# Kernel optimization log

Hardware: AMD Instinct MI355X
Metric: run time of the kernel (lower is better)

Reference implementation:

```python
import jax, jax.numpy as jnp
import numpy as np

N = 100000
E = 1600000
IN_C, HID_C, OUT_C = 64, 64, 16


def setup_inputs() -> dict:
    key = jax.random.key(0)
    k1, k2, k3, k4, k5 = jax.random.split(key, 5)
    x = jax.random.normal(k1, (N, IN_C), dtype=jnp.float32)
    edge_index = jax.random.randint(k2, (2, E), 0, N, dtype=jnp.int64)
    # Glorot-style init like PyG GCNConv
    W1 = jax.random.normal(k3, (IN_C, HID_C), dtype=jnp.float32) * (1.0 / np.sqrt(IN_C))
    b1 = jnp.zeros((HID_C,), dtype=jnp.float32)
    W2 = jax.random.normal(k4, (HID_C, OUT_C), dtype=jnp.float32) * (1.0 / np.sqrt(HID_C))
    b2 = jnp.zeros((OUT_C,), dtype=jnp.float32)
    return {"x": x, "edge_index": edge_index, "W1": W1, "b1": b1, "W2": W2, "b2": b2}


def _gcn_conv(h, src, dst, norm, W, b, n_nodes):
    # h: [N, F_in] -> linear transform first (PyG order), then normalized aggregation
    h = h @ W  # [N, F_out]
    msgs = h[src] * norm[:, None]          # gather + scale, [E+N, F_out]
    out = jax.ops.segment_sum(msgs, dst, num_segments=n_nodes)  # scatter-add
    return out + b


def reference(x, edge_index, W1, b1, W2, b2):
    n = x.shape[0]
    loop = jnp.arange(n, dtype=edge_index.dtype)
    src = jnp.concatenate([edge_index[0], loop])  # add self-loops
    dst = jnp.concatenate([edge_index[1], loop])
    # symmetric normalization D^{-1/2} (A+I) D^{-1/2}
    deg = jax.ops.segment_sum(jnp.ones_like(dst, dtype=x.dtype), dst, num_segments=n)
    dinv = jnp.where(deg > 0, jax.lax.rsqrt(deg), 0.0)
    norm = dinv[src] * dinv[dst]  # [E+N]

    h = jax.nn.relu(_gcn_conv(x, src, dst, norm, W1, b1, n))
    # dropout is identity in eval mode
    return _gcn_conv(h, src, dst, norm, W2, b2, n)
```

## Files before the change

### kernel.cpp

```cpp
#include <hip/hip_runtime.h>


namespace {
constexpr int BLK = 256;
constexpr int NPB = 256;
constexpr int PCHUNK = 2048;
constexpr int STRIDE = 5120;

__device__ inline float bf2f(unsigned short h) {
    union { unsigned u; float f; } v; v.u = (unsigned)h << 16; return v.f;
}
__device__ inline unsigned short f2bf(float f) {
    union { float f; unsigned u; } v; v.f = f;
    unsigned r = (v.u + 0x7FFFu + ((v.u >> 16) & 1u)) >> 16;
    return (unsigned short)r;
}
__device__ inline unsigned pack2bf(float a, float b) {
    return (unsigned)f2bf(a) | ((unsigned)f2bf(b) << 16);
}

__global__ __launch_bounds__(BLK) void k_zero(int* __restrict__ p, int n) {
    int i = blockIdx.x * BLK + threadIdx.x;
    if (i < n) p[i] = 0;
}

__global__ __launch_bounds__(BLK) void k_part(const int* __restrict__ src,
                                              const int* __restrict__ dst,
                                              int* __restrict__ bcnt,
                                              unsigned* __restrict__ packed,
                                              int e, int nb) {
    __shared__ int sdst[PCHUNK];
    __shared__ int hist[1024];
    __shared__ int base[1024];
    int t = threadIdx.x;
    int chunk0 = blockIdx.x * PCHUNK;
    if (chunk0 >= e) return;
    int lim = min(PCHUNK, e - chunk0);
    for (int i = t; i < nb; i += BLK) hist[i] = 0;
    __syncthreads();
    for (int i = t; i < lim; i += BLK) {
        int d = dst[chunk0 + i];
        sdst[i] = d;
        atomicAdd(&hist[d >> 8], 1);
    }
    __syncthreads();
    for (int i = t; i < nb; i += BLK) {
        int c = hist[i];
        base[i] = c ? (i * STRIDE + atomicAdd(&bcnt[i], c)) : 0;
        hist[i] = 0;
    }
    __syncthreads();
    for (int i = t; i < lim; i += BLK) {
        int d = sdst[i];
        int b = d >> 8;
        int r = atomicAdd(&hist[b], 1);
        packed[base[b] + r] = ((unsigned)src[chunk0 + i] << 8) | (unsigned)(d & 255);
    }
}

__global__ __launch_bounds__(BLK) void k_sort(const unsigned* __restrict__ packed,
                                              const int* __restrict__ bcnt,
                                              int* __restrict__ ssrc,
                                              int* __restrict__ rowbeg,
                                              int* __restrict__ rowcnt,
                                              float* __restrict__ dinv, int n) {
    __shared__ int cnt[NPB];
    __shared__ int offs[NPB];
    int b = blockIdx.x;
    int t = threadIdx.x;
    int regionBase = b * STRIDE;
    int ecnt = bcnt[b];
    cnt[t] = 0;
    __syncthreads();
    for (int i = t; i < ecnt; i += BLK) atomicAdd(&cnt[packed[regionBase + i] & 255u], 1);
    __syncthreads();
    int v = cnt[t];
    offs[t] = v;
    __syncthreads();
    for (int off = 1; off < NPB; off <<= 1) {
        int x = (t >= off) ? offs[t - off] : 0;
        __syncthreads();
        offs[t] += x;
        __syncthreads();
    }
    int myoff = offs[t] - v;
    int node = (b << 8) + t;
    if (node < n) {
        rowbeg[node] = regionBase + myoff;
        rowcnt[node] = v;
        dinv[node] = rsqrtf((float)(v + 1));
    }
    __syncthreads();
    cnt[t] = regionBase + myoff;
    __syncthreads();
    for (int i = t; i < ecnt; i += BLK) {
        unsigned p = packed[regionBase + i];
        int pos = atomicAdd(&cnt[p & 255u], 1);
        ssrc[pos] = (int)(p >> 8);
    }
}


__global__ __launch_bounds__(BLK) void k_gemm1(const float* __restrict__ x,
                                               const float* __restrict__ W1,
                                               const float* __restrict__ dinv,
                                               unsigned short* __restrict__ hhat, int n) {
    __shared__ float W[64 * 64];
    int t = threadIdx.x;
    #pragma unroll
    for (int i = 0; i < 16; ++i) W[t + BLK * i] = W1[t + BLK * i];
    __syncthreads();
    const int cg = t & 3;
    const int ng = t >> 2;
    const int node0 = blockIdx.x * 256 + ng * 4;
    const float* Wc = W + cg * 16;

    int nd[4];
    #pragma unroll
    for (int i = 0; i < 4; ++i) {
        int v = node0 + i;
        nd[i] = (v < n) ? v : (n - 1);
    }

    float4 acc[4][4];
    #pragma unroll
    for (int i = 0; i < 4; ++i)
        #pragma unroll
        for (int c = 0; c < 4; ++c) acc[i][c] = make_float4(0.f, 0.f, 0.f, 0.f);

    for (int k4 = 0; k4 < 16; ++k4) {
        float4 xv[4];
        #pragma unroll
        for (int i = 0; i < 4; ++i)
            xv[i] = ((const float4*)(x + (size_t)nd[i] * 64))[k4];
        #pragma unroll
        for (int kk = 0; kk < 4; ++kk) {
            const float4* wr = (const float4*)(Wc + (k4 * 4 + kk) * 64);
            float4 w0 = wr[0], w1 = wr[1], w2 = wr[2], w3 = wr[3];
            #pragma unroll
            for (int i = 0; i < 4; ++i) {
                float xa[4] = {xv[i].x, xv[i].y, xv[i].z, xv[i].w};
                float xs = xa[kk];
                acc[i][0].x = fmaf(xs, w0.x, acc[i][0].x);
                acc[i][0].y = fmaf(xs, w0.y, acc[i][0].y);
                acc[i][0].z = fmaf(xs, w0.z, acc[i][0].z);
                acc[i][0].w = fmaf(xs, w0.w, acc[i][0].w);
                acc[i][1].x = fmaf(xs, w1.x, acc[i][1].x);
                acc[i][1].y = fmaf(xs, w1.y, acc[i][1].y);
                acc[i][1].z = fmaf(xs, w1.z, acc[i][1].z);
                acc[i][1].w = fmaf(xs, w1.w, acc[i][1].w);
                acc[i][2].x = fmaf(xs, w2.x, acc[i][2].x);
                acc[i][2].y = fmaf(xs, w2.y, acc[i][2].y);
                acc[i][2].z = fmaf(xs, w2.z, acc[i][2].z);
                acc[i][2].w = fmaf(xs, w2.w, acc[i][2].w);
                acc[i][3].x = fmaf(xs, w3.x, acc[i][3].x);
                acc[i][3].y = fmaf(xs, w3.y, acc[i][3].y);
                acc[i][3].z = fmaf(xs, w3.z, acc[i][3].z);
                acc[i][3].w = fmaf(xs, w3.w, acc[i][3].w);
            }
        }
    }
    #pragma unroll
    for (int i = 0; i < 4; ++i) {
        int v = node0 + i;
        if (v < n) {
            float d = dinv[v];
            unsigned u0 = pack2bf(acc[i][0].x * d, acc[i][0].y * d);
            unsigned u1 = pack2bf(acc[i][0].z * d, acc[i][0].w * d);
            unsigned u2 = pack2bf(acc[i][1].x * d, acc[i][1].y * d);
            unsigned u3 = pack2bf(acc[i][1].z * d, acc[i][1].w * d);
            unsigned u4 = pack2bf(acc[i][2].x * d, acc[i][2].y * d);
            unsigned u5 = pack2bf(acc[i][2].z * d, acc[i][2].w * d);
            unsigned u6 = pack2bf(acc[i][3].x * d, acc[i][3].y * d);
            unsigned u7 = pack2bf(acc[i][3].z * d, acc[i][3].w * d);
            uint4* dst = (uint4*)(hhat + (size_t)v * 64 + cg * 16);
            dst[0] = make_uint4(u0, u1, u2, u3);
            dst[1] = make_uint4(u4, u5, u6, u7);
        }
    }
}

__global__ __launch_bounds__(BLK) void k_agg1(const unsigned short* __restrict__ hhat,
                                              const int* __restrict__ rowbeg,
                                              const int* __restrict__ rowcnt,
                                              const int* __restrict__ ssrc,
                                              const float* __restrict__ dinv,
                                              const float* __restrict__ b1,
                                              float* __restrict__ h1, int n) {
    int wid = __builtin_amdgcn_readfirstlane(
        (int)((blockIdx.x * BLK + threadIdx.x) >> 6));
    int lane = threadIdx.x & 63;
    if (wid >= n) return;
    int beg = rowbeg[wid];
    int cnt = rowcnt[wid];
    float a = bf2f(hhat[((size_t)wid << 6) + lane]);
    int e = 0;
    for (; e + 8 <= cnt; e += 8) {
        int s0 = ssrc[beg + e + 0], s1 = ssrc[beg + e + 1];
        int s2 = ssrc[beg + e + 2], s3 = ssrc[beg + e + 3];
        int s4 = ssrc[beg + e + 4], s5 = ssrc[beg + e + 5];
        int s6 = ssrc[beg + e + 6], s7 = ssrc[beg + e + 7];
        float v0 = bf2f(hhat[((size_t)s0 << 6) + lane]);
        float v1 = bf2f(hhat[((size_t)s1 << 6) + lane]);
        float v2 = bf2f(hhat[((size_t)s2 << 6) + lane]);
        float v3 = bf2f(hhat[((size_t)s3 << 6) + lane]);
        float v4 = bf2f(hhat[((size_t)s4 << 6) + lane]);
        float v5 = bf2f(hhat[((size_t)s5 << 6) + lane]);
        float v6 = bf2f(hhat[((size_t)s6 << 6) + lane]);
        float v7 = bf2f(hhat[((size_t)s7 << 6) + lane]);
        a += ((v0 + v1) + (v2 + v3)) + ((v4 + v5) + (v6 + v7));
    }
    if (e + 4 <= cnt) {
        int s0 = ssrc[beg + e + 0], s1 = ssrc[beg + e + 1];
        int s2 = ssrc[beg + e + 2], s3 = ssrc[beg + e + 3];
        float v0 = bf2f(hhat[((size_t)s0 << 6) + lane]);
        float v1 = bf2f(hhat[((size_t)s1 << 6) + lane]);
        float v2 = bf2f(hhat[((size_t)s2 << 6) + lane]);
        float v3 = bf2f(hhat[((size_t)s3 << 6) + lane]);
        a += (v0 + v1) + (v2 + v3);
        e += 4;
    }
    for (; e < cnt; ++e)
        a += bf2f(hhat[((size_t)ssrc[beg + e] << 6) + lane]);
    h1[((size_t)wid << 6) + lane] = fmaxf(fmaf(dinv[wid], a, b1[lane]), 0.f);
}

__global__ __launch_bounds__(BLK) void k_gemm2(const float* __restrict__ h1,
                                               const float* __restrict__ W2,
                                               const float* __restrict__ dinv,
                                               unsigned short* __restrict__ h2hat, int n) {
    __shared__ float W[64 * 16];
    int t = threadIdx.x;
    #pragma unroll
    for (int i = 0; i < 4; ++i) W[t + BLK * i] = W2[t + BLK * i];
    __syncthreads();
    int node = blockIdx.x * BLK + t;
    if (node >= n) return;
    const float4* hr = (const float4*)(h1 + (size_t)node * 64);
    float4 a0 = make_float4(0.f, 0.f, 0.f, 0.f);
    float4 a1 = a0, a2 = a0, a3 = a0;
    #pragma unroll 4
    for (int c4 = 0; c4 < 16; ++c4) {
        float4 h = hr[c4];
        #pragma unroll
        for (int kk = 0; kk < 4; ++kk) {
            float ha[4] = {h.x, h.y, h.z, h.w};
            float hv = ha[kk];
            const float4* wr = (const float4*)(W + (c4 * 4 + kk) * 16);
            float4 w0 = wr[0], w1 = wr[1], w2 = wr[2], w3 = wr[3];
            a0.x = fmaf(hv, w0.x, a0.x); a0.y = fmaf(hv, w0.y, a0.y);
            a0.z = fmaf(hv, w0.z, a0.z); a0.w = fmaf(hv, w0.w, a0.w);
            a1.x = fmaf(hv, w1.x, a1.x); a1.y = fmaf(hv, w1.y, a1.y);
            a1.z = fmaf(hv, w1.z, a1.z); a1.w = fmaf(hv, w1.w, a1.w);
            a2.x = fmaf(hv, w2.x, a2.x); a2.y = fmaf(hv, w2.y, a2.y);
            a2.z = fmaf(hv, w2.z, a2.z); a2.w = fmaf(hv, w2.w, a2.w);
            a3.x = fmaf(hv, w3.x, a3.x); a3.y = fmaf(hv, w3.y, a3.y);
            a3.z = fmaf(hv, w3.z, a3.z); a3.w = fmaf(hv, w3.w, a3.w);
        }
    }
    float d = dinv[node];
    uint4* dst = (uint4*)(h2hat + (size_t)node * 16);
    dst[0] = make_uint4(pack2bf(a0.x * d, a0.y * d), pack2bf(a0.z * d, a0.w * d),
                        pack2bf(a1.x * d, a1.y * d), pack2bf(a1.z * d, a1.w * d));
    dst[1] = make_uint4(pack2bf(a2.x * d, a2.y * d), pack2bf(a2.z * d, a2.w * d),
                        pack2bf(a3.x * d, a3.y * d), pack2bf(a3.z * d, a3.w * d));
}

__global__ __launch_bounds__(BLK) void k_agg2(const unsigned short* __restrict__ h2hat,
                                              const int* __restrict__ rowbeg,
                                              const int* __restrict__ rowcnt,
                                              const int* __restrict__ ssrc,
                                              const float* __restrict__ dinv,
                                              const float* __restrict__ b2,
                                              float* __restrict__ out, int n) {
    int wid = __builtin_amdgcn_readfirstlane(
        (int)((blockIdx.x * BLK + threadIdx.x) >> 6));
    int lane = threadIdx.x & 63;
    if (wid >= n) return;
    int q = lane >> 4;
    int c = lane & 15;
    int beg = rowbeg[wid];
    int cnt = rowcnt[wid];
    float a = 0.f;
    int e = q;
    for (; e + 4 < cnt; e += 8) {
        int sa = ssrc[beg + e];
        int sb = ssrc[beg + e + 4];
        float va = bf2f(h2hat[((size_t)sa << 4) + c]);
        float vb = bf2f(h2hat[((size_t)sb << 4) + c]);
        a += va + vb;
    }
    if (e < cnt) a += bf2f(h2hat[((size_t)ssrc[beg + e] << 4) + c]);
    a += __shfl_xor(a, 16, 64);
    a += __shfl_xor(a, 32, 64);
    if (q == 0) {
        float self = bf2f(h2hat[((size_t)wid << 4) + c]);
        out[((size_t)wid << 4) + c] = fmaf(dinv[wid], a + self, b2[c]);
    }
}

}

extern "C" void kernel_launch(void* const* d_in, const int* in_sizes, int n_in,
                              void* d_out, int out_size, void* d_ws, size_t ws_size,
                              hipStream_t stream) {
    const float* x  = (const float*)d_in[0];
    const int*   ei = (const int*)d_in[1];
    const float* W1 = (const float*)d_in[2];
    const float* b1 = (const float*)d_in[3];
    const float* W2 = (const float*)d_in[4];
    const float* b2 = (const float*)d_in[5];
    float* out = (float*)d_out;

    const int N = in_sizes[0] / 64;
    const int E = in_sizes[1] / 2;
    const int* src = ei;
    const int* dst = ei + E;
    const int nb = (N + NPB - 1) / NPB;

    char* ws = (char*)d_ws;
    size_t off = 0;
    auto alloc = [&](size_t bytes) -> char* {
        char* p = ws + off;
        off = (off + bytes + 255) & ~(size_t)255;
        return p;
    };
    int*            bcnt   = (int*)alloc(1024 * 4);
    int*            rowbeg = (int*)alloc((size_t)N * 4);
    int*            rowcnt = (int*)alloc((size_t)N * 4);
    float*          dinv   = (float*)alloc((size_t)N * 4);
    unsigned*       packed = (unsigned*)alloc((size_t)nb * STRIDE * 4);
    int*            ssrc   = (int*)alloc((size_t)nb * STRIDE * 4);
    unsigned short* hhat   = (unsigned short*)alloc((size_t)N * 64 * 2);
    float*          h1     = (float*)alloc((size_t)N * 64 * 4);
    unsigned short* h2hat  = (unsigned short*)alloc((size_t)N * 16 * 2);

    const int nb_n = (N + BLK - 1) / BLK;
    const int nchunks = (E + PCHUNK - 1) / PCHUNK;
    const int nb_w = (int)(((long long)N * 64 + BLK - 1) / BLK);

    k_zero<<<(nb + BLK - 1) / BLK, BLK, 0, stream>>>(bcnt, nb);
    k_part<<<nchunks, BLK, 0, stream>>>(src, dst, bcnt, packed, E, nb);
    k_sort<<<nb, BLK, 0, stream>>>(packed, bcnt, ssrc, rowbeg, rowcnt, dinv, N);

    k_gemm1<<<nb_n, BLK, 0, stream>>>(x, W1, dinv, hhat, N);
    k_agg1<<<nb_w, BLK, 0, stream>>>(hhat, rowbeg, rowcnt, ssrc, dinv, b1, h1, N);

    k_gemm2<<<nb_n, BLK, 0, stream>>>(h1, W2, dinv, h2hat, N);
    k_agg2<<<nb_w, BLK, 0, stream>>>(h2hat, rowbeg, rowcnt, ssrc, dinv, b2, out, N);
}
```

Before: 242.5 us.

## Widen aggregation loads to packed bf16 pairs, pad bucket counters, enlarge sort blocks

The two aggregation kernels now read two bf16 values per 32-bit load. agg1 splits the wave into two halves that each handle alternate edges, and agg2 uses eight slots of eight lanes. Both combine partial sums with cross-lane shuffles. Partition chunks grow fourfold, global bucket counters are padded to separate cache lines to reduce atomic contention, and the sort kernel runs 1024-thread blocks. These changes aim to cut gather instruction count and atomic hot spots, at the cost of extra shuffles, fewer partition blocks, and idle threads in the scan.

Measured after the change: 242.6 us. About the same (+0.0%).

```diff
diff --git a/kernel.cpp b/kernel.cpp
--- a/kernel.cpp
+++ b/kernel.cpp
@@ -4,11 +4,18 @@
 namespace {
 constexpr int BLK = 256;
 constexpr int NPB = 256;
-constexpr int PCHUNK = 2048;
+constexpr int PCHUNK = 8192;
 constexpr int STRIDE = 5120;
+constexpr int CPAD = 32;
 
 __device__ inline float bf2f(unsigned short h) {
     union { unsigned u; float f; } v; v.u = (unsigned)h << 16; return v.f;
+}
+__device__ inline float bfl(unsigned u) {
+    union { unsigned u; float f; } v; v.u = u << 16; return v.f;
+}
+__device__ inline float bfh(unsigned u) {
+    union { unsigned u; float f; } v; v.u = u & 0xFFFF0000u; return v.f;
 }
 __device__ inline unsigned short f2bf(float f) {
     union { float f; unsigned u; } v; v.f = f;
@@ -46,7 +53,7 @@
     __syncthreads();
     for (int i = t; i < nb; i += BLK) {
         int c = hist[i];
-        base[i] = c ? (i * STRIDE + atomicAdd(&bcnt[i], c)) : 0;
+        base[i] = c ? (i * STRIDE + atomicAdd(&bcnt[i * CPAD], c)) : 0;
         hist[i] = 0;
     }
     __syncthreads();
@@ -58,42 +65,47 @@
     }
 }
 
-__global__ __launch_bounds__(BLK) void k_sort(const unsigned* __restrict__ packed,
-                                              const int* __restrict__ bcnt,
-                                              int* __restrict__ ssrc,
-                                              int* __restrict__ rowbeg,
-                                              int* __restrict__ rowcnt,
-                                              float* __restrict__ dinv, int n) {
+__global__ __launch_bounds__(1024) void k_sort(const unsigned* __restrict__ packed,
+                                               const int* __restrict__ bcnt,
+                                               int* __restrict__ ssrc,
+                                               int* __restrict__ rowbeg,
+                                               int* __restrict__ rowcnt,
+                                               float* __restrict__ dinv, int n) {
     __shared__ int cnt[NPB];
     __shared__ int offs[NPB];
     int b = blockIdx.x;
     int t = threadIdx.x;
     int regionBase = b * STRIDE;
-    int ecnt = bcnt[b];
-    cnt[t] = 0;
-    __syncthreads();
-    for (int i = t; i < ecnt; i += BLK) atomicAdd(&cnt[packed[regionBase + i] & 255u], 1);
-    __syncthreads();
-    int v = cnt[t];
-    offs[t] = v;
+    int ecnt = bcnt[b * CPAD];
+    if (t < NPB) cnt[t] = 0;
+    __syncthreads();
+    for (int i = t; i < ecnt; i += 1024)
+        atomicAdd(&cnt[packed[regionBase + i] & 255u], 1);
+    __syncthreads();
+    if (t < NPB) offs[t] = cnt[t];
     __syncthreads();
     for (int off = 1; off < NPB; off <<= 1) {
-        int x = (t >= off) ? offs[t - off] : 0;
+        int x = 0;
+        if (t < NPB && t >= off) x = offs[t - off];
         __syncthreads();
-        offs[t] += x;
+        if (t < NPB) offs[t] += x;
         __syncthreads();
     }
-    int myoff = offs[t] - v;
-    int node = (b << 8) + t;
-    if (node < n) {
-        rowbeg[node] = regionBase + myoff;
-        rowcnt[node] = v;
-        dinv[node] = rsqrtf((float)(v + 1));
-    }
-    __syncthreads();
-    cnt[t] = regionBase + myoff;
-    __syncthreads();
-    for (int i = t; i < ecnt; i += BLK) {
+    int myoff = 0;
+    if (t < NPB) {
+        int v = cnt[t];
+        myoff = offs[t] - v;
+        int node = (b << 8) + t;
+        if (node < n) {
+            rowbeg[node] = regionBase + myoff;
+            rowcnt[node] = v;
+            dinv[node] = rsqrtf((float)(v + 1));
+        }
+    }
+    __syncthreads();
+    if (t < NPB) cnt[t] = regionBase + myoff;
+    __syncthreads();
+    for (int i = t; i < ecnt; i += 1024) {
         unsigned p = packed[regionBase + i];
         int pos = atomicAdd(&cnt[p & 255u], 1);
         ssrc[pos] = (int)(p >> 8);
@@ -180,7 +192,7 @@
     }
 }
 
-__global__ __launch_bounds__(BLK) void k_agg1(const unsigned short* __restrict__ hhat,
+__global__ __launch_bounds__(BLK) void k_agg1(const unsigned* __restrict__ hh,
                                               const int* __restrict__ rowbeg,
                                               const int* __restrict__ rowcnt,
                                               const int* __restrict__ ssrc,
@@ -191,38 +203,49 @@
         (int)((blockIdx.x * BLK + threadIdx.x) >> 6));
     int lane = threadIdx.x & 63;
     if (wid >= n) return;
+    int half = lane >> 5;
+    int cp = lane & 31;
     int beg = rowbeg[wid];
     int cnt = rowcnt[wid];
-    float a = bf2f(hhat[((size_t)wid << 6) + lane]);
+    float ax = 0.f, ay = 0.f;
+    if (half == 0) {
+        unsigned u = hh[((size_t)wid << 5) + cp];
+        ax = bfl(u); ay = bfh(u);
+    }
     int e = 0;
     for (; e + 8 <= cnt; e += 8) {
-        int s0 = ssrc[beg + e + 0], s1 = ssrc[beg + e + 1];
-        int s2 = ssrc[beg + e + 2], s3 = ssrc[beg + e + 3];
-        int s4 = ssrc[beg + e + 4], s5 = ssrc[beg + e + 5];
-        int s6 = ssrc[beg + e + 6], s7 = ssrc[beg + e + 7];
-        float v0 = bf2f(hhat[((size_t)s0 << 6) + lane]);
-        float v1 = bf2f(hhat[((size_t)s1 << 6) + lane]);
-        float v2 = bf2f(hhat[((size_t)s2 << 6) + lane]);
-        float v3 = bf2f(hhat[((size_t)s3 << 6) + lane]);
-        float v4 = bf2f(hhat[((size_t)s4 << 6) + lane]);
-        float v5 = bf2f(hhat[((size_t)s5 << 6) + lane]);
-        float v6 = bf2f(hhat[((size_t)s6 << 6) + lane]);
-        float v7 = bf2f(hhat[((size_t)s7 << 6) + lane]);
-        a += ((v0 + v1) + (v2 + v3)) + ((v4 + v5) + (v6 + v7));
-    }
-    if (e + 4 <= cnt) {
-        int s0 = ssrc[beg + e + 0], s1 = ssrc[beg + e + 1];
-        int s2 = ssrc[beg + e + 2], s3 = ssrc[beg + e + 3];
-        float v0 = bf2f(hhat[((size_t)s0 << 6) + lane]);
-        float v1 = bf2f(hhat[((size_t)s1 << 6) + lane]);
-        float v2 = bf2f(hhat[((size_t)s2 << 6) + lane]);
-        float v3 = bf2f(hhat[((size_t)s3 << 6) + lane]);
-        a += (v0 + v1) + (v2 + v3);
-        e += 4;
-    }
-    for (; e < cnt; ++e)
-        a += bf2f(hhat[((size_t)ssrc[beg + e] << 6) + lane]);
-    h1[((size_t)wid << 6) + lane] = fmaxf(fmaf(dinv[wid], a, b1[lane]), 0.f);
+        int i0 = beg + e + half;
+        int s0 = ssrc[i0];
+        int s1 = ssrc[i0 + 2];
+        int s2 = ssrc[i0 + 4];
+        int s3 = ssrc[i0 + 6];
+        unsigned u0 = hh[((size_t)s0 << 5) + cp];
+        unsigned u1 = hh[((size_t)s1 << 5) + cp];
+        unsigned u2 = hh[((size_t)s2 << 5) + cp];
+        unsigned u3 = hh[((size_t)s3 << 5) + cp];
+        ax += (bfl(u0) + bfl(u1)) + (bfl(u2) + bfl(u3));
+        ay += (bfh(u0) + bfh(u1)) + (bfh(u2) + bfh(u3));
+    }
+    for (; e + 2 <= cnt; e += 2) {
+        int s = ssrc[beg + e + half];
+        unsigned u = hh[((size_t)s << 5) + cp];
+        ax += bfl(u); ay += bfh(u);
+    }
+    if (e < cnt && half == 0) {
+        int s = ssrc[beg + e];
+        unsigned u = hh[((size_t)s << 5) + cp];
+        ax += bfl(u); ay += bfh(u);
+    }
+    ax += __shfl_xor(ax, 32, 64);
+    ay += __shfl_xor(ay, 32, 64);
+    if (half == 0) {
+        float d = dinv[wid];
+        float2 bb = ((const float2*)b1)[cp];
+        float2 o;
+        o.x = fmaxf(fmaf(d, ax, bb.x), 0.f);
+        o.y = fmaxf(fmaf(d, ay, bb.y), 0.f);
+        ((float2*)(h1 + ((size_t)wid << 6)))[cp] = o;
+    }
 }
 
 __global__ __launch_bounds__(BLK) void k_gemm2(const float* __restrict__ h1,
@@ -266,7 +289,7 @@
                         pack2bf(a3.x * d, a3.y * d), pack2bf(a3.z * d, a3.w * d));
 }
 
-__global__ __launch_bounds__(BLK) void k_agg2(const unsigned short* __restrict__ h2hat,
+__global__ __launch_bounds__(BLK) void k_agg2(const unsigned* __restrict__ h2,
                                               const int* __restrict__ rowbeg,
                                               const int* __restrict__ rowcnt,
                                               const int* __restrict__ ssrc,
@@ -277,25 +300,43 @@
         (int)((blockIdx.x * BLK + threadIdx.x) >> 6));
     int lane = threadIdx.x & 63;
     if (wid >= n) return;
-    int q = lane >> 4;
-    int c = lane & 15;
+    int slot = lane >> 3;
+    int u = lane & 7;
     int beg = rowbeg[wid];
     int cnt = rowcnt[wid];
-    float a = 0.f;
-    int e = q;
-    for (; e + 4 < cnt; e += 8) {
-        int sa = ssrc[beg + e];
-        int sb = ssrc[beg + e + 4];
-        float va = bf2f(h2hat[((size_t)sa << 4) + c]);
-        float vb = bf2f(h2hat[((size_t)sb << 4) + c]);
-        a += va + vb;
-    }
-    if (e < cnt) a += bf2f(h2hat[((size_t)ssrc[beg + e] << 4) + c]);
-    a += __shfl_xor(a, 16, 64);
-    a += __shfl_xor(a, 32, 64);
-    if (q == 0) {
-        float self = bf2f(h2hat[((size_t)wid << 4) + c]);
-        out[((size_t)wid << 4) + c] = fmaf(dinv[wid], a + self, b2[c]);
+    float ax = 0.f, ay = 0.f;
+    int e = 0;
+    for (; e + 16 <= cnt; e += 16) {
+        int i0 = beg + e + slot;
+        int s0 = ssrc[i0];
+        int s1 = ssrc[i0 + 8];
+        unsigned u0 = h2[((size_t)s0 << 3) + u];
+        unsigned u1 = h2[((size_t)s1 << 3) + u];
+        ax += bfl(u0) + bfl(u1);
+        ay += bfh(u0) + bfh(u1);
+    }
+    if (e + 8 <= cnt) {
+        int s = ssrc[beg + e + slot];
+        unsigned uu = h2[((size_t)s << 3) + u];
+        ax += bfl(uu); ay += bfh(uu);
+        e += 8;
+    }
+    if (e + slot < cnt) {
+        int s = ssrc[beg + e + slot];
+        unsigned uu = h2[((size_t)s << 3) + u];
+        ax += bfl(uu); ay += bfh(uu);
+    }
+    ax += __shfl_xor(ax, 8, 64);  ay += __shfl_xor(ay, 8, 64);
+    ax += __shfl_xor(ax, 16, 64); ay += __shfl_xor(ay, 16, 64);
+    ax += __shfl_xor(ax, 32, 64); ay += __shfl_xor(ay, 32, 64);
+    if (slot == 0) {
+        unsigned su = h2[((size_t)wid << 3) + u];
+        float d = dinv[wid];
+        float2 bb = ((const float2*)b2)[u];
+        float2 o;
+        o.x = fmaf(d, ax + bfl(su), bb.x);
+        o.y = fmaf(d, ay + bfh(su), bb.y);
+        ((float2*)(out + ((size_t)wid << 4)))[u] = o;
     }
 }
 
@@ -325,7 +366,7 @@
         off = (off + bytes + 255) & ~(size_t)255;
         return p;
     };
-    int*            bcnt   = (int*)alloc(1024 * 4);
+    int*            bcnt   = (int*)alloc((size_t)1024 * CPAD * 4);
     int*            rowbeg = (int*)alloc((size_t)N * 4);
     int*            rowcnt = (int*)alloc((size_t)N * 4);
     float*          dinv   = (float*)alloc((size_t)N * 4);
@@ -339,13 +380,16 @@
     const int nchunks = (E + PCHUNK - 1) / PCHUNK;
     const int nb_w = (int)(((long long)N * 64 + BLK - 1) / BLK);
 
-    k_zero<<<(nb + BLK - 1) / BLK, BLK, 0, stream>>>(bcnt, nb);
+    const int zn = nb * CPAD;
+    k_zero<<<(zn + BLK - 1) / BLK, BLK, 0, stream>>>(bcnt, zn);
     k_part<<<nchunks, BLK, 0, stream>>>(src, dst, bcnt, packed, E, nb);
-    k_sort<<<nb, BLK, 0, stream>>>(packed, bcnt, ssrc, rowbeg, rowcnt, dinv, N);
+    k_sort<<<nb, 1024, 0, stream>>>(packed, bcnt, ssrc, rowbeg, rowcnt, dinv, N);
 
     k_gemm1<<<nb_n, BLK, 0, stream>>>(x, W1, dinv, hhat, N);
-    k_agg1<<<nb_w, BLK, 0, stream>>>(hhat, rowbeg, rowcnt, ssrc, dinv, b1, h1, N);
+    k_agg1<<<nb_w, BLK, 0, stream>>>((const unsigned*)hhat, rowbeg, rowcnt, ssrc,
+                                     dinv, b1, h1, N);
 
     k_gemm2<<<nb_n, BLK, 0, stream>>>(h1, W2, dinv, h2hat, N);
-    k_agg2<<<nb_w, BLK, 0, stream>>>(h2hat, rowbeg, rowcnt, ssrc, dinv, b2, out, N);
-}
+    k_agg2<<<nb_w, BLK, 0, stream>>>((const unsigned*)h2hat, rowbeg, rowcnt, ssrc,
+                                     dinv, b2, out, N);
+}
```

## Fuse second GEMM into layer-1 aggregation, vectorize partitioning, pad bucket counters

Applied to the files above, without the earlier changes.

The layer-2 linear transform now happens inside the layer-1 aggregation kernel, using wave shuffles against W2 columns held in registers. This removes the fp32 h1 intermediate round trip and one kernel launch. The partition kernel reads src/dst as int4, and the global bucket counters are padded to separate cache lines to cut atomic contention. The sort kernel runs 512 threads and stages the bucket in LDS so it reads global memory once, and agg2 changes how lanes take edges. Risks are int4 loads assuming alignment, and extra register and shuffle work in agg1.

Result: no change. 241.5 us (-0.4%).

```diff
diff --git a/kernel.cpp b/kernel.cpp
--- a/kernel.cpp
+++ b/kernel.cpp
@@ -6,6 +6,7 @@
 constexpr int NPB = 256;
 constexpr int PCHUNK = 2048;
 constexpr int STRIDE = 5120;
+constexpr int CPAD = 32;
 
 __device__ inline float bf2f(unsigned short h) {
     union { unsigned u; float f; } v; v.u = (unsigned)h << 16; return v.f;
@@ -36,9 +37,19 @@
     int chunk0 = blockIdx.x * PCHUNK;
     if (chunk0 >= e) return;
     int lim = min(PCHUNK, e - chunk0);
+    int lim4 = lim >> 2;
     for (int i = t; i < nb; i += BLK) hist[i] = 0;
     __syncthreads();
-    for (int i = t; i < lim; i += BLK) {
+    const int4* d4 = (const int4*)(dst + chunk0);
+    for (int i = t; i < lim4; i += BLK) {
+        int4 d = d4[i];
+        ((int4*)sdst)[i] = d;
+        atomicAdd(&hist[d.x >> 8], 1);
+        atomicAdd(&hist[d.y >> 8], 1);
+        atomicAdd(&hist[d.z >> 8], 1);
+        atomicAdd(&hist[d.w >> 8], 1);
+    }
+    for (int i = (lim4 << 2) + t; i < lim; i += BLK) {
         int d = dst[chunk0 + i];
         sdst[i] = d;
         atomicAdd(&hist[d >> 8], 1);
@@ -46,11 +57,25 @@
     __syncthreads();
     for (int i = t; i < nb; i += BLK) {
         int c = hist[i];
-        base[i] = c ? (i * STRIDE + atomicAdd(&bcnt[i], c)) : 0;
+        base[i] = c ? (i * STRIDE + atomicAdd(&bcnt[i * CPAD], c)) : 0;
         hist[i] = 0;
     }
     __syncthreads();
-    for (int i = t; i < lim; i += BLK) {
+    const int4* s4 = (const int4*)(src + chunk0);
+    for (int i = t; i < lim4; i += BLK) {
+        int4 d = ((int4*)sdst)[i];
+        int4 s = s4[i];
+        int b0 = d.x >> 8, b1 = d.y >> 8, b2 = d.z >> 8, b3 = d.w >> 8;
+        int r0 = atomicAdd(&hist[b0], 1);
+        packed[base[b0] + r0] = ((unsigned)s.x << 8) | (unsigned)(d.x & 255);
+        int r1 = atomicAdd(&hist[b1], 1);
+        packed[base[b1] + r1] = ((unsigned)s.y << 8) | (unsigned)(d.y & 255);
+        int r2 = atomicAdd(&hist[b2], 1);
+        packed[base[b2] + r2] = ((unsigned)s.z << 8) | (unsigned)(d.z & 255);
+        int r3 = atomicAdd(&hist[b3], 1);
+        packed[base[b3] + r3] = ((unsigned)s.w << 8) | (unsigned)(d.w & 255);
+    }
+    for (int i = (lim4 << 2) + t; i < lim; i += BLK) {
         int d = sdst[i];
         int b = d >> 8;
         int r = atomicAdd(&hist[b], 1);
@@ -58,43 +83,52 @@
     }
 }
 
-__global__ __launch_bounds__(BLK) void k_sort(const unsigned* __restrict__ packed,
+__global__ __launch_bounds__(512) void k_sort(const unsigned* __restrict__ packed,
                                               const int* __restrict__ bcnt,
                                               int* __restrict__ ssrc,
                                               int* __restrict__ rowbeg,
                                               int* __restrict__ rowcnt,
                                               float* __restrict__ dinv, int n) {
+    __shared__ unsigned sp[STRIDE];
     __shared__ int cnt[NPB];
     __shared__ int offs[NPB];
     int b = blockIdx.x;
     int t = threadIdx.x;
     int regionBase = b * STRIDE;
-    int ecnt = bcnt[b];
-    cnt[t] = 0;
-    __syncthreads();
-    for (int i = t; i < ecnt; i += BLK) atomicAdd(&cnt[packed[regionBase + i] & 255u], 1);
-    __syncthreads();
-    int v = cnt[t];
-    offs[t] = v;
+    int ecnt = bcnt[b * CPAD];
+    if (t < NPB) cnt[t] = 0;
+    __syncthreads();
+    for (int i = t; i < ecnt; i += 512) {
+        unsigned p = packed[regionBase + i];
+        sp[i] = p;
+        atomicAdd(&cnt[p & 255u], 1);
+    }
+    __syncthreads();
+    if (t < NPB) offs[t] = cnt[t];
     __syncthreads();
     for (int off = 1; off < NPB; off <<= 1) {
-        int x = (t >= off) ? offs[t - off] : 0;
+        int x = 0;
+        if (t < NPB && t >= off) x = offs[t - off];
         __syncthreads();
-        offs[t] += x;
+        if (t < NPB) offs[t] += x;
         __syncthreads();
     }
-    int myoff = offs[t] - v;
-    int node = (b << 8) + t;
-    if (node < n) {
-        rowbeg[node] = regionBase + myoff;
-        rowcnt[node] = v;
-        dinv[node] = rsqrtf((float)(v + 1));
-    }
-    __syncthreads();
-    cnt[t] = regionBase + myoff;
-    __syncthreads();
-    for (int i = t; i < ecnt; i += BLK) {
-        unsigned p = packed[regionBase + i];
+    int myoff = 0;
+    if (t < NPB) {
+        int v = cnt[t];
+        myoff = offs[t] - v;
+        int node = (b << 8) + t;
+        if (node < n) {
+            rowbeg[node] = regionBase + myoff;
+            rowcnt[node] = v;
+            dinv[node] = rsqrtf((float)(v + 1));
+        }
+    }
+    __syncthreads();
+    if (t < NPB) cnt[t] = regionBase + myoff;
+    __syncthreads();
+    for (int i = t; i < ecnt; i += 512) {
+        unsigned p = sp[i];
         int pos = atomicAdd(&cnt[p & 255u], 1);
         ssrc[pos] = (int)(p >> 8);
     }
@@ -186,11 +220,18 @@
                                               const int* __restrict__ ssrc,
                                               const float* __restrict__ dinv,
                                               const float* __restrict__ b1,
-                                              float* __restrict__ h1, int n) {
+                                              const float* __restrict__ W2,
+                                              unsigned short* __restrict__ h2hat, int n) {
     int wid = __builtin_amdgcn_readfirstlane(
         (int)((blockIdx.x * BLK + threadIdx.x) >> 6));
     int lane = threadIdx.x & 63;
     if (wid >= n) return;
+    const int g = lane >> 4;
+    const int j = lane & 15;
+    float w2r[16];
+    #pragma unroll
+    for (int k = 0; k < 16; ++k) w2r[k] = W2[(g * 16 + k) * 16 + j];
+
     int beg = rowbeg[wid];
     int cnt = rowcnt[wid];
     float a = bf2f(hhat[((size_t)wid << 6) + lane]);
@@ -222,51 +263,22 @@
     }
     for (; e < cnt; ++e)
         a += bf2f(hhat[((size_t)ssrc[beg + e] << 6) + lane]);
-    h1[((size_t)wid << 6) + lane] = fmaxf(fmaf(dinv[wid], a, b1[lane]), 0.f);
-}
-
-__global__ __launch_bounds__(BLK) void k_gemm2(const float* __restrict__ h1,
-                                               const float* __restrict__ W2,
-                                               const float* __restrict__ dinv,
-                                               unsigned short* __restrict__ h2hat, int n) {
-    __shared__ float W[64 * 16];
-    int t = threadIdx.x;
-    #pragma unroll
-    for (int i = 0; i < 4; ++i) W[t + BLK * i] = W2[t + BLK * i];
-    __syncthreads();
-    int node = blockIdx.x * BLK + t;
-    if (node >= n) return;
-    const float4* hr = (const float4*)(h1 + (size_t)node * 64);
-    float4 a0 = make_float4(0.f, 0.f, 0.f, 0.f);
-    float4 a1 = a0, a2 = a0, a3 = a0;
-    #pragma unroll 4
-    for (int c4 = 0; c4 < 16; ++c4) {
-        float4 h = hr[c4];
-        #pragma unroll
-        for (int kk = 0; kk < 4; ++kk) {
-            float ha[4] = {h.x, h.y, h.z, h.w};
-            float hv = ha[kk];
-            const float4* wr = (const float4*)(W + (c4 * 4 + kk) * 16);
-            float4 w0 = wr[0], w1 = wr[1], w2 = wr[2], w3 = wr[3];
-            a0.x = fmaf(hv, w0.x, a0.x); a0.y = fmaf(hv, w0.y, a0.y);
-            a0.z = fmaf(hv, w0.z, a0.z); a0.w = fmaf(hv, w0.w, a0.w);
-            a1.x = fmaf(hv, w1.x, a1.x); a1.y = fmaf(hv, w1.y, a1.y);
-            a1.z = fmaf(hv, w1.z, a1.z); a1.w = fmaf(hv, w1.w, a1.w);
-            a2.x = fmaf(hv, w2.x, a2.x); a2.y = fmaf(hv, w2.y, a2.y);
-            a2.z = fmaf(hv, w2.z, a2.z); a2.w = fmaf(hv, w2.w, a2.w);
-            a3.x = fmaf(hv, w3.x, a3.x); a3.y = fmaf(hv, w3.y, a3.y);
-            a3.z = fmaf(hv, w3.z, a3.z); a3.w = fmaf(hv, w3.w, a3.w);
-        }
-    }
-    float d = dinv[node];
-    uint4* dst = (uint4*)(h2hat + (size_t)node * 16);
-    dst[0] = make_uint4(pack2bf(a0.x * d, a0.y * d), pack2bf(a0.z * d, a0.w * d),
-                        pack2bf(a1.x * d, a1.y * d), pack2bf(a1.z * d, a1.w * d));
-    dst[1] = make_uint4(pack2bf(a2.x * d, a2.y * d), pack2bf(a2.z * d, a2.w * d),
-                        pack2bf(a3.x * d, a3.y * d), pack2bf(a3.z * d, a3.w * d));
-}
-
-__global__ __launch_bounds__(BLK) void k_agg2(const unsigned short* __restrict__ h2hat,
+
+    float dv = dinv[wid];
+    float h = fmaxf(fmaf(dv, a, b1[lane]), 0.f);
+
+    float part = 0.f;
+    #pragma unroll
+    for (int k = 0; k < 16; ++k) {
+        float hv = __shfl(h, g * 16 + k, 64);
+        part = fmaf(hv, w2r[k], part);
+    }
+    part += __shfl_xor(part, 16, 64);
+    part += __shfl_xor(part, 32, 64);
+    if (g == 0) h2hat[(size_t)wid * 16 + j] = f2bf(part * dv);
+}
+
+__global__ __launch_bounds__(BLK) void k_agg2(const unsigned short* __restrict__ h2,
                                               const int* __restrict__ rowbeg,
                                               const int* __restrict__ rowcnt,
                                               const int* __restrict__ ssrc,
@@ -282,19 +294,21 @@
     int beg = rowbeg[wid];
     int cnt = rowcnt[wid];
     float a = 0.f;
-    int e = q;
-    for (; e + 4 < cnt; e += 8) {
-        int sa = ssrc[beg + e];
-        int sb = ssrc[beg + e + 4];
-        float va = bf2f(h2hat[((size_t)sa << 4) + c]);
-        float vb = bf2f(h2hat[((size_t)sb << 4) + c]);
-        a += va + vb;
-    }
-    if (e < cnt) a += bf2f(h2hat[((size_t)ssrc[beg + e] << 4) + c]);
+    int e = 0;
+    for (; e + 4 <= cnt; e += 4) {
+        int s0 = ssrc[beg + e + 0], s1 = ssrc[beg + e + 1];
+        int s2 = ssrc[beg + e + 2], s3 = ssrc[beg + e + 3];
+        int sa = (q & 1) ? s1 : s0;
+        int sb = (q & 1) ? s3 : s2;
+        int s = (q & 2) ? sb : sa;
+        a += bf2f(h2[((size_t)s << 4) + c]);
+    }
+    if (e + q < cnt)
+        a += bf2f(h2[((size_t)ssrc[beg + e + q] << 4) + c]);
     a += __shfl_xor(a, 16, 64);
     a += __shfl_xor(a, 32, 64);
     if (q == 0) {
-        float self = bf2f(h2hat[((size_t)wid << 4) + c]);
+        float self = bf2f(h2[((size_t)wid << 4) + c]);
         out[((size_t)wid << 4) + c] = fmaf(dinv[wid], a + self, b2[c]);
     }
 }
@@ -325,27 +339,26 @@
         off = (off + bytes + 255) & ~(size_t)255;
         return p;
     };
-    int*            bcnt   = (int*)alloc(1024 * 4);
+    int*            bcnt   = (int*)alloc((size_t)1024 * CPAD * 4);
     int*            rowbeg = (int*)alloc((size_t)N * 4);
     int*            rowcnt = (int*)alloc((size_t)N * 4);
     float*          dinv   = (float*)alloc((size_t)N * 4);
     unsigned*       packed = (unsigned*)alloc((size_t)nb * STRIDE * 4);
     int*            ssrc   = (int*)alloc((size_t)nb * STRIDE * 4);
     unsigned short* hhat   = (unsigned short*)alloc((size_t)N * 64 * 2);
-    float*          h1     = (float*)alloc((size_t)N * 64 * 4);
     unsigned short* h2hat  = (unsigned short*)alloc((size_t)N * 16 * 2);
 
     const int nb_n = (N + BLK - 1) / BLK;
     const int nchunks = (E + PCHUNK - 1) / PCHUNK;
     const int nb_w = (int)(((long long)N * 64 + BLK - 1) / BLK);
 
-    k_zero<<<(nb + BLK - 1) / BLK, BLK, 0, stream>>>(bcnt, nb);
+    const int zn = nb * CPAD;
+    k_zero<<<(zn + BLK - 1) / BLK, BLK, 0, stream>>>(bcnt, zn);
     k_part<<<nchunks, BLK, 0, stream>>>(src, dst, bcnt, packed, E, nb);
-    k_sort<<<nb, BLK, 0, stream>>>(packed, bcnt, ssrc, rowbeg, rowcnt, dinv, N);
+    k_sort<<<nb, 512, 0, stream>>>(packed, bcnt, ssrc, rowbeg, rowcnt, dinv, N);
 
     k_gemm1<<<nb_n, BLK, 0, stream>>>(x, W1, dinv, hhat, N);
-    k_agg1<<<nb_w, BLK, 0, stream>>>(hhat, rowbeg, rowcnt, ssrc, dinv, b1, h1, N);
-
-    k_gemm2<<<nb_n, BLK, 0, stream>>>(h1, W2, dinv, h2hat, N);
+    k_agg1<<<nb_w, BLK, 0, stream>>>(hhat, rowbeg, rowcnt, ssrc, dinv, b1, W2,
+                                     h2hat, N);
     k_agg2<<<nb_w, BLK, 0, stream>>>(h2hat, rowbeg, rowcnt, ssrc, dinv, b2, out, N);
 }
```
